# Kernel tuning notes

Measured on AMD Instinct MI355X. Metric: run time of the kernel, lower is better.

Reference implementation:

```python
import jax, jax.numpy as jnp
import numpy as np

NODE_TYPES = ["patient", "visit", "symptom", "procedure", "disease", "drug"]
N = {"patient": 20000, "visit": 100000, "symptom": 4000, "procedure": 8000,
     "disease": 10000, "drug": 4000}
D = 128          # embedding_dim == hidden_channels
N_LAYERS = 4     # conv1..conv4
# (src, dst) per relation; reverse edges included so every node type gets messages
REL = [("patient", "visit"), ("visit", "patient"),
       ("visit", "symptom"), ("symptom", "visit"),
       ("visit", "procedure"), ("procedure", "visit"),
       ("visit", "disease"), ("disease", "visit"),
       ("visit", "drug"), ("drug", "visit")]
E_FWD = {("patient", "visit"): 100000, ("visit", "symptom"): 300000,
         ("visit", "procedure"): 200000, ("visit", "disease"): 250000,
         ("visit", "drug"): 300000}
EI_NAMES = ["ei_pv", "ei_vp", "ei_vs", "ei_sv", "ei_vpr", "ei_prv",
            "ei_vd", "ei_dv", "ei_vdr", "ei_drv"]
E_LABEL = 200000


def setup_inputs() -> dict:
    key = jax.random.key(0)
    ks = iter(jax.random.split(key, 64))
    inp = {}
    for nt in NODE_TYPES:
        inp[f"node_id_{nt}"] = jnp.arange(N[nt], dtype=jnp.int32)
        inp[f"emb_{nt}"] = jax.random.normal(next(ks), (N[nt], D), jnp.float32)
    for name, (src, dst) in zip(EI_NAMES, REL):
        e = E_FWD.get((src, dst), E_FWD.get((dst, src)))
        row = jax.random.randint(next(ks), (e,), 0, N[src], dtype=jnp.int32)
        col = jax.random.randint(next(ks), (e,), 0, N[dst], dtype=jnp.int32)
        inp[name] = jnp.stack([row, col])
    R = len(REL)
    inp["W_l"] = jax.random.normal(next(ks), (N_LAYERS, R, D, D), jnp.float32) * 0.05
    inp["b_l"] = jnp.zeros((N_LAYERS, R, D), jnp.float32)
    inp["W_r"] = jax.random.normal(next(ks), (N_LAYERS, R, D, D), jnp.float32) * 0.05
    inp["cls_w1"] = jax.random.normal(next(ks), (2 * D, D), jnp.float32) * 0.05
    inp["cls_b1"] = jnp.zeros((D,), jnp.float32)
    inp["cls_w2"] = jax.random.normal(next(ks), (D, 1), jnp.float32) * 0.05
    inp["cls_b2"] = jnp.zeros((1,), jnp.float32)
    row = jax.random.randint(next(ks), (E_LABEL,), 0, N["visit"], dtype=jnp.int32)
    col = jax.random.randint(next(ks), (E_LABEL,), 0, N["drug"], dtype=jnp.int32)
    inp["edge_label_index"] = jnp.stack([row, col])
    inp["edge_label"] = jax.random.bernoulli(next(ks), 0.5, (E_LABEL,)).astype(jnp.float32)
    return inp


def _hetero_sage_layer(x, eis, Wl, bl, Wr):
    # to_hetero semantics: out[dst] = sum over edge types (src,rel,dst) of
    #   SAGEConv_rel: lin_l(mean_j x[src][j]) + lin_r(x[dst])   (PyG defaults)
    out = {nt: jnp.zeros_like(v) for nt, v in x.items()}
    for r, (src, dst) in enumerate(REL):
        ei = eis[r]
        n_dst = x[dst].shape[0]
        msg = jax.ops.segment_sum(x[src][ei[0]], ei[1], num_segments=n_dst)
        deg = jax.ops.segment_sum(jnp.ones((ei.shape[1],), x[src].dtype), ei[1],
                                  num_segments=n_dst)
        mean = msg / jnp.maximum(deg, 1.0)[:, None]  # empty segments stay 0 as in PyG
        out[dst] = out[dst] + mean @ Wl[r] + bl[r] + x[dst] @ Wr[r]
    return out


def reference(node_id_patient, node_id_visit, node_id_symptom, node_id_procedure,
              node_id_disease, node_id_drug,
              emb_patient, emb_visit, emb_symptom, emb_procedure, emb_disease, emb_drug,
              ei_pv, ei_vp, ei_vs, ei_sv, ei_vpr, ei_prv, ei_vd, ei_dv, ei_vdr, ei_drv,
              W_l, b_l, W_r, cls_w1, cls_b1, cls_w2, cls_b2,
              edge_label_index, edge_label):
    x = {"patient": emb_patient[node_id_patient],
         "visit": emb_visit[node_id_visit],
         "symptom": emb_symptom[node_id_symptom],
         "procedure": emb_procedure[node_id_procedure],
         "disease": emb_disease[node_id_disease],
         "drug": emb_drug[node_id_drug]}
    eis = [ei_pv, ei_vp, ei_vs, ei_sv, ei_vpr, ei_prv, ei_vd, ei_dv, ei_vdr, ei_drv]
    for l in range(N_LAYERS):
        x = _hetero_sage_layer(x, eis, W_l[l], b_l[l], W_r[l])
        if l < N_LAYERS - 1:  # relu after conv1..conv3 only; dropout is eval-mode identity
            x = {k: jax.nn.relu(v) for k, v in x.items()}
    # Classifier: gather visit/drug node features per labeled edge, concat, MLP
    zv = x["visit"][edge_label_index[0]]
    zd = x["drug"][edge_label_index[1]]
    h = jax.nn.relu(jnp.concatenate([zv, zd], axis=-1) @ cls_w1 + cls_b1)
    pred = (h @ cls_w2 + cls_b2).reshape(-1)
    # BCE with logits: softplus(z) - z*y, mean-reduced
    loss = jnp.mean(jax.nn.softplus(pred) - pred * edge_label)
    return loss, pred
```

## Files before the change

### kernel.cpp

```cpp
#include <hip/hip_runtime.h>
#include <cmath>


typedef _Float16 f16x8 __attribute__((ext_vector_type(8)));
typedef float f32x4 __attribute__((ext_vector_type(4)));

#define NREL 10
#define NCOUNTS 546000
#define NEDGES  2300000
#define NVISIT  100000
#define NVEDGES 1150000
#define PLW 546816
#define WT_ELEMS (4 * PLW + 69632)
#define XELEMS 18688000UL
#define SELEMS 5888000UL
#define NBKT 873
#define BCAP 5056

struct GatherMeta { const float* emb[6]; const int* nid[6]; int rows[6]; int off[6]; };
struct AggMeta { const int* rp[5]; _Float16* meanH[5]; _Float16* meanL[5]; int M[5]; };
struct BkMeta {
  const int* ei[NREL]; int E[NREL]; int cbc[NREL]; int ndst[NREL];
  int sh[NREL]; int bb[NREL]; int nb[NREL];
};
struct MTask {
  const _Float16* AH0; const _Float16* AL0;
  const _Float16* AH1; const _Float16* AL1;
  const _Float16* W;
  const float* bias;
  _Float16* outH; _Float16* outL;
  int M, blkOff, K, relu;
};
struct MMeta { MTask t[6]; int nTasks; };

__global__ __launch_bounds__(256) void conv0(GatherMeta g, _Float16* __restrict__ H,
                                             _Float16* __restrict__ L) {
  int t = blockIdx.y;
  int i = blockIdx.x * 256 + threadIdx.x;
  if (i >= g.rows[t] * 16) return;
  int row = i >> 4, q = i & 15;
  int s = g.nid[t][row];
  const float* p = g.emb[t] + (size_t)s * 128 + q * 8;
  float4 v0 = *(const float4*)p;
  float4 v1 = *(const float4*)(p + 4);
  float v[8] = {v0.x, v0.y, v0.z, v0.w, v1.x, v1.y, v1.z, v1.w};
  f16x8 h, l;
  #pragma unroll
  for (int j = 0; j < 8; ++j) {
    h[j] = (_Float16)v[j];
    l[j] = (_Float16)(v[j] - (float)h[j]);
  }
  size_t o = (size_t)(g.off[t] + row) * 128 + q * 8;
  *(f16x8*)(H + o) = h;
  *(f16x8*)(L + o) = l;
}

__global__ __launch_bounds__(256) void bkt_p1(BkMeta bm, int* __restrict__ bcur,
                                              int* __restrict__ bdata) {
  __shared__ int cnt[128];
  __shared__ int base[128];
  __shared__ unsigned short rnk[4096];
  int r = blockIdx.y;
  int E = bm.E[r], sh = bm.sh[r], bb = bm.bb[r], nb = bm.nb[r];
  int tid = threadIdx.x;
  if (tid < 128) cnt[tid] = 0;
  __syncthreads();
  int e0 = blockIdx.x * 4096;
  if (e0 >= E) return;
  const int* dstp = bm.ei[r] + E;
  const int* srcp = bm.ei[r];
  #pragma unroll
  for (int i = 0; i < 16; ++i) {
    int e = e0 + i * 256 + tid;
    if (e < E) {
      int b = dstp[e] >> sh;
      rnk[i * 256 + tid] = (unsigned short)atomicAdd(&cnt[b], 1);
    }
  }
  __syncthreads();
  if (tid < nb && cnt[tid] > 0) base[tid] = atomicAdd(&bcur[bb + tid], cnt[tid]);
  __syncthreads();
  #pragma unroll
  for (int i = 0; i < 16; ++i) {
    int e = e0 + i * 256 + tid;
    if (e < E) {
      int d = dstp[e];
      int b = d >> sh;
      int pos = base[b] + (int)rnk[i * 256 + tid];
      if (pos < BCAP)
        bdata[(size_t)(bb + b) * BCAP + pos] = ((d & ((1 << sh) - 1)) << 17) | srcp[e];
    }
  }
}

__global__ __launch_bounds__(256) void bkt_p2a(BkMeta bm, const int* __restrict__ bcur,
                                               const int* __restrict__ bdata,
                                               int* __restrict__ counts) {
  __shared__ int hist[2048];
  int g = blockIdx.x;
  int r = 0;
  #pragma unroll
  for (int i = 1; i < NREL; ++i) if (g >= bm.bb[i]) r = i;
  int lb = g - bm.bb[r];
  int sh = bm.sh[r], dpb = 1 << sh;
  int tid = threadIdx.x;
  for (int d = tid; d < dpb; d += 256) hist[d] = 0;
  __syncthreads();
  int cnt = bcur[g]; if (cnt > BCAP) cnt = BCAP;
  const int* bd = bdata + (size_t)g * BCAP;
  for (int i = tid; i < cnt; i += 256) atomicAdd(&hist[((unsigned)bd[i]) >> 17], 1);
  __syncthreads();
  int dBase = lb << sh;
  int dMax = bm.ndst[r] - dBase; if (dMax > dpb) dMax = dpb;
  for (int d = tid; d < dMax; d += 256) counts[bm.cbc[r] + dBase + d] = hist[d];
}

__global__ __launch_bounds__(1024) void scan1(const int* __restrict__ counts,
                                              int* __restrict__ partials) {
  __shared__ int s[1024];
  int i = blockIdx.x * 1024 + threadIdx.x;
  s[threadIdx.x] = (i < NCOUNTS) ? counts[i] : 0;
  __syncthreads();
  for (int off = 512; off > 0; off >>= 1) {
    if (threadIdx.x < off) s[threadIdx.x] += s[threadIdx.x + off];
    __syncthreads();
  }
  if (threadIdx.x == 0) partials[blockIdx.x] = s[0];
}

__global__ __launch_bounds__(1024) void scan2(int* __restrict__ partials, int nb) {
  __shared__ int s[1024];
  int t = threadIdx.x;
  int v = (t < nb) ? partials[t] : 0;
  s[t] = v;
  __syncthreads();
  for (int off = 1; off < 1024; off <<= 1) {
    int add = (t >= off) ? s[t - off] : 0;
    __syncthreads();
    s[t] += add;
    __syncthreads();
  }
  if (t < nb) partials[t] = s[t] - v;
}

__global__ __launch_bounds__(1024) void scan3(const int* __restrict__ counts,
                                              int* __restrict__ prefix,
                                              const int* __restrict__ partials) {
  __shared__ int s[1024];
  int t = threadIdx.x;
  int i = blockIdx.x * 1024 + t;
  int v = (i < NCOUNTS) ? counts[i] : 0;
  s[t] = v;
  __syncthreads();
  for (int off = 1; off < 1024; off <<= 1) {
    int add = (t >= off) ? s[t - off] : 0;
    __syncthreads();
    s[t] += add;
    __syncthreads();
  }
  int P = partials[blockIdx.x] + s[t] - v;
  if (i < NCOUNTS) prefix[i] = P;
  if (blockIdx.x == 0 && t == 0) prefix[NCOUNTS] = NEDGES;
}

__global__ __launch_bounds__(256) void bkt_p2b(BkMeta bm, const int* __restrict__ bcur,
                                               const int* __restrict__ bdata,
                                               const int* __restrict__ prefix,
                                               int* __restrict__ esrc) {
  __shared__ int pk[BCAP];
  __shared__ int srt[BCAP];
  __shared__ int cur[2048];
  __shared__ int part[256];
  __shared__ int baseSh;
  int g = blockIdx.x;
  int r = 0;
  #pragma unroll
  for (int i = 1; i < NREL; ++i) if (g >= bm.bb[i]) r = i;
  int lb = g - bm.bb[r];
  int sh = bm.sh[r], dpb = 1 << sh;
  int tid = threadIdx.x;
  int cnt = bcur[g]; if (cnt > BCAP) cnt = BCAP;
  const int* bd = bdata + (size_t)g * BCAP;
  for (int d = tid; d < dpb; d += 256) cur[d] = 0;
  for (int i = tid; i < cnt; i += 256) pk[i] = bd[i];
  __syncthreads();
  for (int i = tid; i < cnt; i += 256) atomicAdd(&cur[((unsigned)pk[i]) >> 17], 1);
  __syncthreads();
  int seg = (dpb + 255) >> 8;
  int s = 0;
  int b0 = tid * seg;
  for (int j = 0; j < seg; ++j) {
    int idx = b0 + j;
    if (idx < dpb) { int v = cur[idx]; cur[idx] = s; s += v; }
  }
  part[tid] = s;
  __syncthreads();
  for (int off = 1; off < 256; off <<= 1) {
    int add = (tid >= off) ? part[tid - off] : 0;
    __syncthreads();
    part[tid] += add;
    __syncthreads();
  }
  int myoff = part[tid] - s;
  for (int j = 0; j < seg; ++j) {
    int idx = b0 + j;
    if (idx < dpb) cur[idx] += myoff;
  }
  if (tid == 0) baseSh = prefix[bm.cbc[r] + (lb << sh)];
  __syncthreads();
  for (int i = tid; i < cnt; i += 256) {
    int p = pk[i];
    int pos = atomicAdd(&cur[((unsigned)p) >> 17], 1);
    srt[pos] = p & 0x1FFFF;
  }
  __syncthreads();
  int base = baseSh;
  for (int i = tid; i < cnt; i += 256) esrc[base + i] = srt[i];
}

__global__ __launch_bounds__(256) void merge_visit(const int* __restrict__ prefix,
                                                   const int* __restrict__ esrc,
                                                   int* __restrict__ mprefix,
                                                   int2* __restrict__ mesrc) {
  const int cbc[5]  = {0, 124000, 232000, 342000, 446000};
  const int yoff[5] = {0, 20000, 24000, 32000, 42000};
  int v = blockIdx.x * 256 + threadIdx.x;
  if (v >= NVISIT) return;
  int e0[5], e1[5];
  int base = 0;
  #pragma unroll
  for (int q = 0; q < 5; ++q) {
    e0[q] = prefix[cbc[q] + v];
    e1[q] = prefix[cbc[q] + v + 1];
    base += e0[q] - prefix[cbc[q]];
  }
  mprefix[v] = base;
  if (v == NVISIT - 1) {
    int t = base;
    #pragma unroll
    for (int q = 0; q < 5; ++q) t += e1[q] - e0[q];
    mprefix[NVISIT] = t;
  }
  int pos = base;
  #pragma unroll
  for (int q = 0; q < 5; ++q) {
    int d = e1[q] - e0[q];
    if (d > 0) {
      int wb = __float_as_int(1.f / (float)d);
      for (int e = e0[q]; e < e1[q]; ++e)
        mesrc[pos++] = make_int2(yoff[q] + esrc[e], wb);
    }
  }
}

__global__ __launch_bounds__(256) void prep_split(
    const float* __restrict__ W_l, const float* __restrict__ b_l,
    const float* __restrict__ W_r, const float* __restrict__ cw1,
    _Float16* __restrict__ Wt, float* __restrict__ visitSumB) {
  const int visitRel[5] = {0, 3, 5, 7, 9};
  const int inRel[5] = {1, 2, 4, 6, 8};
  int gid = blockIdx.x * 256 + threadIdx.x;
  if (gid < 1048576) {
    int l = gid >> 18, o = gid & 262143;
    float val; size_t base; int n, k, Kpad;
    if (o < 163840) {
      int t = o >> 15, e = o & 32767;
      k = e >> 7; n = e & 127; Kpad = 264;
      int r = inRel[t];
      val = (k < 128) ? W_l[(size_t)(l * 10 + r) * 16384 + k * 128 + n]
                      : W_r[(size_t)(l * 10 + r) * 16384 + (k - 128) * 128 + n];
      base = (size_t)l * PLW + t * 67584;
    } else if (o < 245760) {
      int q = (o - 163840) >> 14, e = (o - 163840) & 16383;
      k = e >> 7; n = e & 127; Kpad = 136;
      val = W_l[(size_t)(l * 10 + visitRel[q]) * 16384 + k * 128 + n];
      base = (size_t)l * PLW + 337920 + q * 34816;
    } else {
      int e = o - 245760;
      k = e >> 7; n = e & 127; Kpad = 136;
      val = 0.f;
      #pragma unroll
      for (int q = 0; q < 5; ++q)
        val += W_r[(size_t)(l * 10 + visitRel[q]) * 16384 + k * 128 + n];
      base = (size_t)l * PLW + 512000;
    }
    _Float16 h = (_Float16)val;
    _Float16 lo = (_Float16)(val - (float)h);
    Wt[base + (size_t)n * Kpad + k] = h;
    Wt[base + (size_t)(128 + n) * Kpad + k] = lo;
  } else if (gid < 1081344) {
    int e = gid - 1048576;
    int k = e >> 7, n = e & 127;
    float val = cw1[(size_t)k * 128 + n];
    _Float16 h = (_Float16)val;
    _Float16 lo = (_Float16)(val - (float)h);
    size_t base = (size_t)4 * PLW + (k < 128 ? 0 : 34816);
    int kk = k & 127;
    Wt[base + (size_t)n * 136 + kk] = h;
    Wt[base + (size_t)(128 + n) * 136 + kk] = lo;
  } else if (gid < 1081856) {
    int e = gid - 1081344;
    int l = e >> 7, c = e & 127;
    float val = 0.f;
    #pragma unroll
    for (int q = 0; q < 5; ++q) val += b_l[(l * 10 + visitRel[q]) * 128 + c];
    visitSumB[e] = val;
  }
}

__global__ __launch_bounds__(256) void agg_small(AggMeta m,
                                                 const _Float16* __restrict__ xvH,
                                                 const int* __restrict__ esrc) {
  int t = blockIdx.y;
  int row = blockIdx.x * 16 + (threadIdx.x >> 4);
  if (row >= m.M[t]) return;
  int q = threadIdx.x & 15;
  const int* rp = m.rp[t];
  int e0 = rp[row], e1 = rp[row + 1];
  float a[8];
  #pragma unroll
  for (int j = 0; j < 8; ++j) a[j] = 0.f;
  int e = e0;
  for (; e + 4 <= e1; e += 4) {
    int s0 = esrc[e], s1 = esrc[e + 1], s2 = esrc[e + 2], s3 = esrc[e + 3];
    f16x8 v0 = *(const f16x8*)(xvH + (size_t)s0 * 128 + q * 8);
    f16x8 v1 = *(const f16x8*)(xvH + (size_t)s1 * 128 + q * 8);
    f16x8 v2 = *(const f16x8*)(xvH + (size_t)s2 * 128 + q * 8);
    f16x8 v3 = *(const f16x8*)(xvH + (size_t)s3 * 128 + q * 8);
    #pragma unroll
    for (int j = 0; j < 8; ++j)
      a[j] += ((float)v0[j] + (float)v1[j]) + ((float)v2[j] + (float)v3[j]);
  }
  for (; e < e1; ++e) {
    int s = esrc[e];
    f16x8 v = *(const f16x8*)(xvH + (size_t)s * 128 + q * 8);
    #pragma unroll
    for (int j = 0; j < 8; ++j) a[j] += (float)v[j];
  }
  float inv = (e1 > e0) ? 1.f / (float)(e1 - e0) : 0.f;
  f16x8 h, l;
  #pragma unroll
  for (int j = 0; j < 8; ++j) {
    float v = a[j] * inv;
    h[j] = (_Float16)v;
    l[j] = (_Float16)(v - (float)h[j]);
  }
  size_t o = (size_t)row * 128 + q * 8;
  *(f16x8*)(m.meanH[t] + o) = h;
  *(f16x8*)(m.meanL[t] + o) = l;
}

__global__ __launch_bounds__(256) void agg_visit(const int* __restrict__ mprefix,
                                                 const int2* __restrict__ mesrc,
                                                 const _Float16* __restrict__ YH,
                                                 _Float16* __restrict__ xvH,
                                                 _Float16* __restrict__ xvL, int doRelu) {
  int row = blockIdx.x * 16 + (threadIdx.x >> 4);
  if (row >= NVISIT) return;
  int q = threadIdx.x & 15;
  size_t o = (size_t)row * 128 + q * 8;
  f16x8 h0 = *(f16x8*)(xvH + o);
  f16x8 l0 = *(f16x8*)(xvL + o);
  float a[8];
  #pragma unroll
  for (int j = 0; j < 8; ++j) a[j] = (float)h0[j] + (float)l0[j];
  int e0 = mprefix[row], e1 = mprefix[row + 1];
  int e = e0;
  for (; e + 4 <= e1; e += 4) {
    int2 p0 = mesrc[e], p1 = mesrc[e + 1], p2 = mesrc[e + 2], p3 = mesrc[e + 3];
    f16x8 v0 = *(const f16x8*)(YH + (size_t)p0.x * 128 + q * 8);
    f16x8 v1 = *(const f16x8*)(YH + (size_t)p1.x * 128 + q * 8);
    f16x8 v2 = *(const f16x8*)(YH + (size_t)p2.x * 128 + q * 8);
    f16x8 v3 = *(const f16x8*)(YH + (size_t)p3.x * 128 + q * 8);
    float w0 = __int_as_float(p0.y), w1 = __int_as_float(p1.y);
    float w2 = __int_as_float(p2.y), w3 = __int_as_float(p3.y);
    #pragma unroll
    for (int j = 0; j < 8; ++j)
      a[j] += (w0 * (float)v0[j] + w1 * (float)v1[j]) +
              (w2 * (float)v2[j] + w3 * (float)v3[j]);
  }
  for (; e < e1; ++e) {
    int2 p = mesrc[e];
    f16x8 v = *(const f16x8*)(YH + (size_t)p.x * 128 + q * 8);
    float w = __int_as_float(p.y);
    #pragma unroll
    for (int j = 0; j < 8; ++j) a[j] += w * (float)v[j];
  }
  f16x8 h, l;
  #pragma unroll
  for (int j = 0; j < 8; ++j) {
    float v = doRelu ? fmaxf(a[j], 0.f) : a[j];
    h[j] = (_Float16)v;
    l[j] = (_Float16)(v - (float)h[j]);
  }
  *(f16x8*)(xvH + o) = h;
  *(f16x8*)(xvL + o) = l;
}

__global__ __launch_bounds__(256, 2) void mgemm(MMeta mm) {
  int b = blockIdx.x;
  int ti = 0;
  for (int i = 1; i < mm.nTasks; ++i) if (b >= mm.t[i].blkOff) ti = i;
  MTask tk = mm.t[ti];
  int blockRow = (b - tk.blkOff) * 128;
  int Kpad = tk.K + 8;

  __shared__ _Float16 Ash[2][128][72];
  int tid = threadIdx.x;
  int wave = tid >> 6, lane = tid & 63;
  int quad = lane >> 4, lm = lane & 15;
  int wr = wave >> 1, wc = wave & 1;

  f32x4 acc[4][4];
  #pragma unroll
  for (int i = 0; i < 4; ++i)
    #pragma unroll
    for (int j = 0; j < 4; ++j) acc[i][j] = (f32x4){0.f, 0.f, 0.f, 0.f};

  const _Float16* wrowH[4];
  const _Float16* wrowL[4];
  #pragma unroll
  for (int nt = 0; nt < 4; ++nt) {
    int n = wc * 64 + nt * 16 + lm;
    wrowH[nt] = tk.W + (size_t)n * Kpad;
    wrowL[nt] = tk.W + (size_t)(128 + n) * Kpad;
  }

  int sr = tid >> 1, sk = (tid & 1) * 32;
  int gr = blockRow + sr; if (gr >= tk.M) gr = tk.M - 1;
  for (int k0 = 0; k0 < tk.K; k0 += 64) {
    const _Float16* AH = (k0 < 128) ? tk.AH0 : tk.AH1;
    const _Float16* AL = (k0 < 128) ? tk.AL0 : tk.AL1;
    size_t abase = (size_t)gr * 128 + (k0 & 127) + sk;
    #pragma unroll
    for (int c = 0; c < 4; ++c) {
      *(f16x8*)&Ash[0][sr][sk + c * 8] = *(const f16x8*)(AH + abase + c * 8);
      *(f16x8*)&Ash[1][sr][sk + c * 8] = *(const f16x8*)(AL + abase + c * 8);
    }
    __syncthreads();
    #pragma unroll
    for (int ks = 0; ks < 64; ks += 32) {
      int kf = k0 + ks + quad * 8;
      f16x8 bh[4], bl[4];
      #pragma unroll
      for (int nt = 0; nt < 4; ++nt) {
        bh[nt] = *(const f16x8*)(wrowH[nt] + kf);
        bl[nt] = *(const f16x8*)(wrowL[nt] + kf);
      }
      #pragma unroll
      for (int mt = 0; mt < 4; ++mt) {
        int r = wr * 64 + mt * 16 + lm;
        f16x8 ah = *(const f16x8*)&Ash[0][r][ks + quad * 8];
        f16x8 al = *(const f16x8*)&Ash[1][r][ks + quad * 8];
        #pragma unroll
        for (int nt = 0; nt < 4; ++nt) {
          acc[mt][nt] = __builtin_amdgcn_mfma_f32_16x16x32_f16(ah, bh[nt], acc[mt][nt], 0, 0, 0);
          acc[mt][nt] = __builtin_amdgcn_mfma_f32_16x16x32_f16(ah, bl[nt], acc[mt][nt], 0, 0, 0);
          acc[mt][nt] = __builtin_amdgcn_mfma_f32_16x16x32_f16(al, bh[nt], acc[mt][nt], 0, 0, 0);
        }
      }
    }
    __syncthreads();
  }

  float bv[4];
  #pragma unroll
  for (int nt = 0; nt < 4; ++nt)
    bv[nt] = tk.bias ? tk.bias[wc * 64 + nt * 16 + lm] : 0.f;
  #pragma unroll
  for (int mt = 0; mt < 4; ++mt) {
    #pragma unroll
    for (int i = 0; i < 4; ++i) {
      int grow = blockRow + wr * 64 + mt * 16 + quad * 4 + i;
      if (grow >= tk.M) continue;
      size_t ob = (size_t)grow * 128 + wc * 64 + lm;
      #pragma unroll
      for (int nt = 0; nt < 4; ++nt) {
        float v = acc[mt][nt][i] + bv[nt];
        if (tk.relu) v = fmaxf(v, 0.f);
        _Float16 h = (_Float16)v;
        tk.outH[ob + nt * 16] = h;
        if (tk.outL) tk.outL[ob + nt * 16] = (_Float16)(v - (float)h);
      }
    }
  }
}

__global__ __launch_bounds__(256) void cls_edge(
    const _Float16* __restrict__ UH, const _Float16* __restrict__ UL,
    const _Float16* __restrict__ VH, const _Float16* __restrict__ VL,
    const int* __restrict__ eli, const float* __restrict__ w2,
    const float* __restrict__ b2, const float* __restrict__ y,
    float* __restrict__ lossOut, float* __restrict__ pred, int M) {
  __shared__ float lsum[4];
  int tid = threadIdx.x;
  int q = tid & 15;
  int lane = tid & 63;
  float w2v[8];
  #pragma unroll
  for (int j = 0; j < 8; ++j) w2v[j] = w2[q * 8 + j];
  float bias = b2[0];
  float lacc = 0.f;
  int e0 = blockIdx.x * 128 + (tid >> 4);
  #pragma unroll
  for (int p = 0; p < 8; ++p) {
    int e = e0 + p * 16;
    if (e < M) {
      int vi = eli[e], di = eli[M + e];
      size_t uo = (size_t)vi * 128 + q * 8;
      size_t vo = (size_t)di * 128 + q * 8;
      f16x8 uh = *(const f16x8*)(UH + uo);
      f16x8 ul = *(const f16x8*)(UL + uo);
      f16x8 vh = *(const f16x8*)(VH + vo);
      f16x8 vl = *(const f16x8*)(VL + vo);
      float part = 0.f;
      #pragma unroll
      for (int j = 0; j < 8; ++j) {
        float t = ((float)uh[j] + (float)ul[j]) + ((float)vh[j] + (float)vl[j]);
        part += fmaxf(t, 0.f) * w2v[j];
      }
      part += __shfl_xor(part, 1);
      part += __shfl_xor(part, 2);
      part += __shfl_xor(part, 4);
      part += __shfl_xor(part, 8);
      if (q == 0) {
        float z = part + bias;
        pred[e] = z;
        lacc += fmaxf(z, 0.f) + log1pf(expf(-fabsf(z))) - z * y[e];
      }
    }
  }
  lacc += __shfl_xor(lacc, 16);
  lacc += __shfl_xor(lacc, 32);
  if (lane == 0) lsum[tid >> 6] = lacc;
  __syncthreads();
  if (tid == 0)
    atomicAdd(lossOut, (lsum[0] + lsum[1] + lsum[2] + lsum[3]) * (1.0f / 200000.0f));
}

extern "C" void kernel_launch(void* const* d_in, const int* in_sizes, int n_in,
                              void* d_out, int out_size, void* d_ws, size_t ws_size,
                              hipStream_t stream) {
  static const int kRows[6] = {20000, 100000, 4000, 8000, 10000, 4000};
  static const int kOff[6]  = {0, 20000, 120000, 124000, 132000, 142000};
  static const int kSmallT[5]   = {0, 2, 3, 4, 5};
  static const int kInRel[5]    = {1, 2, 4, 6, 8};
  static const int kCbcIn[5]    = {100000, 120000, 224000, 332000, 442000};
  static const int kYOff[5]     = {0, 20000, 24000, 32000, 42000};
  static const int kBOff[5]     = {0, 157, 189, 252, 331};
  static const int kCbcA[NREL]  = {0, 100000, 120000, 124000, 224000,
                                   232000, 332000, 342000, 442000, 446000};
  static const int kEhA[NREL]   = {100000, 100000, 300000, 300000, 200000,
                                   200000, 250000, 250000, 300000, 300000};
  static const int kNdst[NREL]  = {100000, 20000, 4000, 100000, 8000,
                                   100000, 10000, 100000, 4000, 100000};
  static const int kSh[NREL]    = {11, 9, 5, 10, 7, 10, 7, 10, 5, 10};
  static const int kNB[NREL]    = {49, 40, 125, 98, 63, 98, 79, 98, 125, 98};
  static const int kBB[NREL]    = {0, 49, 89, 214, 312, 375, 473, 552, 650, 775};

  const float* W_l = (const float*)d_in[22];
  const float* b_l = (const float*)d_in[23];
  const float* W_r = (const float*)d_in[24];
  const float* cw1 = (const float*)d_in[25];
  const float* cb1 = (const float*)d_in[26];
  const float* cw2 = (const float*)d_in[27];
  const float* cb2 = (const float*)d_in[28];
  const int* eli = (const int*)d_in[29];
  const float* ylab = (const float*)d_in[30];

  _Float16* H = (_Float16*)d_ws;
  _Float16* L = H + XELEMS;
  _Float16* meanH = L + XELEMS;
  _Float16* meanL = meanH + SELEMS;
  _Float16* YH = meanL + SELEMS;
  _Float16* Wt = YH + SELEMS;
  int* prefix = (int*)(Wt + WT_ELEMS);
  int* counts = prefix + 546004;
  int* esrc = counts + NCOUNTS;
  int* partials = esrc + NEDGES;
  float* visitSumB = (float*)(partials + 1024);
  int* bcur = (int*)(visitSumB + 512);
  int* bdata = bcur + 1024;

  int* mprefix = counts;
  int2* mesrc = (int2*)bdata;

  _Float16* UH = meanH;
  _Float16* VH = meanH + (size_t)NVISIT * 128;
  _Float16* VL = VH + (size_t)4000 * 128;
  _Float16* UL = (_Float16*)prefix;

  BkMeta bm;
  for (int r = 0; r < NREL; ++r) {
    bm.ei[r] = (const int*)d_in[12 + r];
    bm.E[r] = kEhA[r];
    bm.cbc[r] = kCbcA[r];
    bm.ndst[r] = kNdst[r];
    bm.sh[r] = kSh[r];
    bm.bb[r] = kBB[r];
    bm.nb[r] = kNB[r];
  }

  hipMemsetAsync(bcur, 0, NBKT * sizeof(int), stream);
  hipMemsetAsync(d_out, 0, sizeof(float), stream);

  prep_split<<<(1081856 + 255) / 256, 256, 0, stream>>>(W_l, b_l, W_r, cw1, Wt, visitSumB);

  GatherMeta gm;
  for (int t = 0; t < 6; ++t) {
    gm.nid[t] = (const int*)d_in[2 * t];
    gm.emb[t] = (const float*)d_in[2 * t + 1];
    gm.rows[t] = kRows[t];
    gm.off[t] = kOff[t];
  }
  conv0<<<dim3(6250, 6), 256, 0, stream>>>(gm, H, L);

  bkt_p1<<<dim3(74, NREL), 256, 0, stream>>>(bm, bcur, bdata);
  bkt_p2a<<<dim3(NBKT), 256, 0, stream>>>(bm, bcur, bdata, counts);
  scan1<<<534, 1024, 0, stream>>>(counts, partials);
  scan2<<<1, 1024, 0, stream>>>(partials, 534);
  scan3<<<534, 1024, 0, stream>>>(counts, prefix, partials);
  bkt_p2b<<<dim3(NBKT), 256, 0, stream>>>(bm, bcur, bdata, prefix, esrc);
  merge_visit<<<dim3((NVISIT + 255) / 256), 256, 0, stream>>>(prefix, esrc, mprefix, mesrc);

  _Float16* xvH = H + (size_t)kOff[1] * 128;
  _Float16* xvL = L + (size_t)kOff[1] * 128;

  for (int l = 0; l < 4; ++l) {
    int doRelu = (l < 3);
    int last = (l == 3);
    _Float16* LW = Wt + (size_t)l * PLW;

    AggMeta am;
    if (!last) {
      for (int t = 0; t < 5; ++t) {
        am.rp[t] = prefix + kCbcIn[t];
        am.meanH[t] = meanH + (size_t)kYOff[t] * 128;
        am.meanL[t] = meanL + (size_t)kYOff[t] * 128;
        am.M[t] = kRows[kSmallT[t]];
      }
      agg_small<<<dim3(1250, 5), 256, 0, stream>>>(am, xvH, esrc);
    } else {
      am.rp[0] = prefix + kCbcIn[4];
      am.meanH[0] = meanH + (size_t)kYOff[4] * 128;
      am.meanL[0] = meanL + (size_t)kYOff[4] * 128;
      am.M[0] = 4000;
      agg_small<<<dim3(250, 1), 256, 0, stream>>>(am, xvH, esrc);
    }

    MMeta m2;
    m2.nTasks = 6;
    for (int q = 0; q < 5; ++q) {
      size_t so = (size_t)kOff[kSmallT[q]] * 128;
      m2.t[q].AH0 = H + so; m2.t[q].AL0 = L + so;
      m2.t[q].AH1 = nullptr; m2.t[q].AL1 = nullptr;
      m2.t[q].W = LW + 337920 + (size_t)q * 34816;
      m2.t[q].bias = nullptr;
      m2.t[q].outH = YH + (size_t)kYOff[q] * 128;
      m2.t[q].outL = nullptr;
      m2.t[q].M = kRows[kSmallT[q]];
      m2.t[q].blkOff = kBOff[q];
      m2.t[q].K = 128;
      m2.t[q].relu = 0;
    }
    m2.t[5].AH0 = xvH; m2.t[5].AL0 = xvL;
    m2.t[5].AH1 = nullptr; m2.t[5].AL1 = nullptr;
    m2.t[5].W = LW + 512000;
    m2.t[5].bias = visitSumB + l * 128;
    m2.t[5].outH = xvH; m2.t[5].outL = xvL;
    m2.t[5].M = NVISIT;
    m2.t[5].blkOff = 363;
    m2.t[5].K = 128;
    m2.t[5].relu = 0;
    mgemm<<<dim3(363 + 782), 256, 0, stream>>>(m2);

    MMeta m1;
    if (!last) {
      m1.nTasks = 5;
      for (int t = 0; t < 5; ++t) {
        size_t mo = (size_t)kYOff[t] * 128;
        size_t so = (size_t)kOff[kSmallT[t]] * 128;
        m1.t[t].AH0 = meanH + mo; m1.t[t].AL0 = meanL + mo;
        m1.t[t].AH1 = H + so;     m1.t[t].AL1 = L + so;
        m1.t[t].W = LW + (size_t)t * 67584;
        m1.t[t].bias = b_l + (size_t)(l * 10 + kInRel[t]) * 128;
        m1.t[t].outH = H + so;    m1.t[t].outL = L + so;
        m1.t[t].M = kRows[kSmallT[t]];
        m1.t[t].blkOff = kBOff[t];
        m1.t[t].K = 256;
        m1.t[t].relu = doRelu;
      }
      mgemm<<<dim3(363), 256, 0, stream>>>(m1);
    } else {
      size_t mo = (size_t)kYOff[4] * 128;
      size_t so = (size_t)kOff[5] * 128;
      m1.nTasks = 1;
      m1.t[0].AH0 = meanH + mo; m1.t[0].AL0 = meanL + mo;
      m1.t[0].AH1 = H + so;     m1.t[0].AL1 = L + so;
      m1.t[0].W = LW + (size_t)4 * 67584;
      m1.t[0].bias = b_l + (size_t)(l * 10 + kInRel[4]) * 128;
      m1.t[0].outH = H + so;    m1.t[0].outL = L + so;
      m1.t[0].M = 4000;
      m1.t[0].blkOff = 0;
      m1.t[0].K = 256;
      m1.t[0].relu = 0;
      mgemm<<<dim3(32), 256, 0, stream>>>(m1);
    }

    agg_visit<<<dim3(6250), 256, 0, stream>>>(mprefix, mesrc, YH, xvH, xvL, doRelu);
  }

  MMeta muv;
  muv.nTasks = 2;
  muv.t[0].AH0 = xvH; muv.t[0].AL0 = xvL;
  muv.t[0].AH1 = nullptr; muv.t[0].AL1 = nullptr;
  muv.t[0].W = Wt + (size_t)4 * PLW;
  muv.t[0].bias = cb1;
  muv.t[0].outH = UH; muv.t[0].outL = UL;
  muv.t[0].M = NVISIT;
  muv.t[0].blkOff = 0;
  muv.t[0].K = 128;
  muv.t[0].relu = 0;
  muv.t[1].AH0 = H + (size_t)kOff[5] * 128; muv.t[1].AL0 = L + (size_t)kOff[5] * 128;
  muv.t[1].AH1 = nullptr; muv.t[1].AL1 = nullptr;
  muv.t[1].W = Wt + (size_t)4 * PLW + 34816;
  muv.t[1].bias = nullptr;
  muv.t[1].outH = VH; muv.t[1].outL = VL;
  muv.t[1].M = 4000;
  muv.t[1].blkOff = 782;
  muv.t[1].K = 128;
  muv.t[1].relu = 0;
  mgemm<<<dim3(782 + 32), 256, 0, stream>>>(muv);

  const int ML = 200000;
  cls_edge<<<dim3((ML + 127) / 128), 256, 0, stream>>>(
      UH, UL, VH, VL, eli, cw2, cb2, ylab,
      (float*)d_out, (float*)d_out + 1, ML);
}
```

Measured before the change: 943.0 us.

## Fuse small-type aggregation with message GEMM; merge visit self-GEMM into update launch

```diff
diff --git a/kernel.cpp b/kernel.cpp
--- a/kernel.cpp
+++ b/kernel.cpp
@@ -18,7 +18,6 @@
 #define BCAP 5056
 
 struct GatherMeta { const float* emb[6]; const int* nid[6]; int rows[6]; int off[6]; };
-struct AggMeta { const int* rp[5]; _Float16* meanH[5]; _Float16* meanL[5]; int M[5]; };
 struct BkMeta {
   const int* ei[NREL]; int E[NREL]; int cbc[NREL]; int ndst[NREL];
   int sh[NREL]; int bb[NREL]; int nb[NREL];
@@ -32,6 +31,12 @@
   int M, blkOff, K, relu;
 };
 struct MMeta { MTask t[6]; int nTasks; };
+struct F1Meta {
+  const int* rp[5]; _Float16* mH[5]; _Float16* mL[5]; int aM[5]; int aOff[5];
+  int nAgg; int aggTotal;
+  const _Float16* gAH[5]; const _Float16* gAL[5]; const _Float16* gW[5];
+  _Float16* gY[5]; int gM[5]; int gOff[5]; int nG;
+};
 
 __global__ __launch_bounds__(256) void conv0(GatherMeta g, _Float16* __restrict__ H,
                                              _Float16* __restrict__ L) {
@@ -308,46 +313,92 @@
   }
 }
 
-__global__ __launch_bounds__(256) void agg_small(AggMeta m,
+__global__ __launch_bounds__(256, 8) void fused1(F1Meta f,
                                                  const _Float16* __restrict__ xvH,
                                                  const int* __restrict__ esrc) {
-  int t = blockIdx.y;
-  int row = blockIdx.x * 16 + (threadIdx.x >> 4);
-  if (row >= m.M[t]) return;
-  int q = threadIdx.x & 15;
-  const int* rp = m.rp[t];
-  int e0 = rp[row], e1 = rp[row + 1];
-  float a[8];
-  #pragma unroll
-  for (int j = 0; j < 8; ++j) a[j] = 0.f;
-  int e = e0;
-  for (; e + 4 <= e1; e += 4) {
-    int s0 = esrc[e], s1 = esrc[e + 1], s2 = esrc[e + 2], s3 = esrc[e + 3];
-    f16x8 v0 = *(const f16x8*)(xvH + (size_t)s0 * 128 + q * 8);
-    f16x8 v1 = *(const f16x8*)(xvH + (size_t)s1 * 128 + q * 8);
-    f16x8 v2 = *(const f16x8*)(xvH + (size_t)s2 * 128 + q * 8);
-    f16x8 v3 = *(const f16x8*)(xvH + (size_t)s3 * 128 + q * 8);
-    #pragma unroll
-    for (int j = 0; j < 8; ++j)
-      a[j] += ((float)v0[j] + (float)v1[j]) + ((float)v2[j] + (float)v3[j]);
-  }
-  for (; e < e1; ++e) {
-    int s = esrc[e];
-    f16x8 v = *(const f16x8*)(xvH + (size_t)s * 128 + q * 8);
-    #pragma unroll
-    for (int j = 0; j < 8; ++j) a[j] += (float)v[j];
-  }
-  float inv = (e1 > e0) ? 1.f / (float)(e1 - e0) : 0.f;
-  f16x8 h, l;
-  #pragma unroll
-  for (int j = 0; j < 8; ++j) {
-    float v = a[j] * inv;
-    h[j] = (_Float16)v;
-    l[j] = (_Float16)(v - (float)h[j]);
-  }
-  size_t o = (size_t)row * 128 + q * 8;
-  *(f16x8*)(m.meanH[t] + o) = h;
-  *(f16x8*)(m.meanL[t] + o) = l;
+  int b = blockIdx.x;
+  int tid = threadIdx.x;
+  if (b < f.aggTotal) {
+    int t = 0;
+    #pragma unroll
+    for (int i = 1; i < 5; ++i) if (i < f.nAgg && b >= f.aOff[i]) t = i;
+    int row = (b - f.aOff[t]) * 16 + (tid >> 4);
+    if (row >= f.aM[t]) return;
+    int q = tid & 15;
+    const int* rp = f.rp[t];
+    int e0 = rp[row], e1 = rp[row + 1];
+    float a[8];
+    #pragma unroll
+    for (int j = 0; j < 8; ++j) a[j] = 0.f;
+    int e = e0;
+    for (; e + 4 <= e1; e += 4) {
+      int s0 = esrc[e], s1 = esrc[e + 1], s2 = esrc[e + 2], s3 = esrc[e + 3];
+      f16x8 v0 = *(const f16x8*)(xvH + (size_t)s0 * 128 + q * 8);
+      f16x8 v1 = *(const f16x8*)(xvH + (size_t)s1 * 128 + q * 8);
+      f16x8 v2 = *(const f16x8*)(xvH + (size_t)s2 * 128 + q * 8);
+      f16x8 v3 = *(const f16x8*)(xvH + (size_t)s3 * 128 + q * 8);
+      #pragma unroll
+      for (int j = 0; j < 8; ++j)
+        a[j] += ((float)v0[j] + (float)v1[j]) + ((float)v2[j] + (float)v3[j]);
+    }
+    for (; e < e1; ++e) {
+      int s = esrc[e];
+      f16x8 v = *(const f16x8*)(xvH + (size_t)s * 128 + q * 8);
+      #pragma unroll
+      for (int j = 0; j < 8; ++j) a[j] += (float)v[j];
+    }
+    float inv = (e1 > e0) ? 1.f / (float)(e1 - e0) : 0.f;
+    f16x8 h, l;
+    #pragma unroll
+    for (int j = 0; j < 8; ++j) {
+      float v = a[j] * inv;
+      h[j] = (_Float16)v;
+      l[j] = (_Float16)(v - (float)h[j]);
+    }
+    size_t o = (size_t)row * 128 + q * 8;
+    *(f16x8*)(f.mH[t] + o) = h;
+    *(f16x8*)(f.mL[t] + o) = l;
+    return;
+  }
+  b -= f.aggTotal;
+  int g = 0;
+  #pragma unroll
+  for (int i = 1; i < 5; ++i) if (i < f.nG && b >= f.gOff[i]) g = i;
+  int blockRow = (b - f.gOff[g]) * 32;
+  int lane = tid & 63, wave = tid >> 6;
+  int quad = lane >> 4, lm = lane & 15;
+  int wr = wave >> 1, wc = wave & 1;
+  const _Float16* AH = f.gAH[g];
+  const _Float16* AL = f.gAL[g];
+  const _Float16* W = f.gW[g];
+  int M = f.gM[g];
+  int ar = blockRow + wr * 16 + lm;
+  if (ar >= M) ar = M - 1;
+  f32x4 acc[4];
+  #pragma unroll
+  for (int nt = 0; nt < 4; ++nt) acc[nt] = (f32x4){0.f, 0.f, 0.f, 0.f};
+  for (int ks = 0; ks < 128; ks += 32) {
+    f16x8 ah = *(const f16x8*)(AH + (size_t)ar * 128 + ks + quad * 8);
+    f16x8 al = *(const f16x8*)(AL + (size_t)ar * 128 + ks + quad * 8);
+    #pragma unroll
+    for (int nt = 0; nt < 4; ++nt) {
+      int n = wc * 64 + nt * 16 + lm;
+      f16x8 bh = *(const f16x8*)(W + (size_t)n * 136 + ks + quad * 8);
+      f16x8 bl = *(const f16x8*)(W + (size_t)(128 + n) * 136 + ks + quad * 8);
+      acc[nt] = __builtin_amdgcn_mfma_f32_16x16x32_f16(ah, bh, acc[nt], 0, 0, 0);
+      acc[nt] = __builtin_amdgcn_mfma_f32_16x16x32_f16(ah, bl, acc[nt], 0, 0, 0);
+      acc[nt] = __builtin_amdgcn_mfma_f32_16x16x32_f16(al, bh, acc[nt], 0, 0, 0);
+    }
+  }
+  _Float16* Y = f.gY[g];
+  #pragma unroll
+  for (int i = 0; i < 4; ++i) {
+    int grow = blockRow + wr * 16 + quad * 4 + i;
+    if (grow >= M) continue;
+    #pragma unroll
+    for (int nt = 0; nt < 4; ++nt)
+      Y[(size_t)grow * 128 + wc * 64 + nt * 16 + lm] = (_Float16)acc[nt][i];
+  }
 }
 
 __global__ __launch_bounds__(256) void agg_visit(const int* __restrict__ mprefix,
@@ -548,6 +599,9 @@
   static const int kCbcIn[5]    = {100000, 120000, 224000, 332000, 442000};
   static const int kYOff[5]     = {0, 20000, 24000, 32000, 42000};
   static const int kBOff[5]     = {0, 157, 189, 252, 331};
+  static const int kAggOff[5]   = {0, 1250, 1500, 2000, 2625};
+  static const int kLeanOff[5]  = {0, 625, 750, 1000, 1313};
+  const int kAggTotal = 2875, kLeanTotal = 1438;
   static const int kCbcA[NREL]  = {0, 100000, 120000, 124000, 224000,
                                    232000, 332000, 342000, 442000, 446000};
   static const int kEhA[NREL]   = {100000, 100000, 300000, 300000, 200000,
@@ -631,80 +685,88 @@
     int last = (l == 3);
     _Float16* LW = Wt + (size_t)l * PLW;
 
-    AggMeta am;
+    F1Meta f1;
     if (!last) {
       for (int t = 0; t < 5; ++t) {
-        am.rp[t] = prefix + kCbcIn[t];
-        am.meanH[t] = meanH + (size_t)kYOff[t] * 128;
-        am.meanL[t] = meanL + (size_t)kYOff[t] * 128;
-        am.M[t] = kRows[kSmallT[t]];
+        f1.rp[t] = prefix + kCbcIn[t];
+        f1.mH[t] = meanH + (size_t)kYOff[t] * 128;
+        f1.mL[t] = meanL + (size_t)kYOff[t] * 128;
+        f1.aM[t] = kRows[kSmallT[t]];
+        f1.aOff[t] = kAggOff[t];
       }
-      agg_small<<<dim3(1250, 5), 256, 0, stream>>>(am, xvH, esrc);
+      f1.nAgg = 5;
+      f1.aggTotal = kAggTotal;
     } else {
-      am.rp[0] = prefix + kCbcIn[4];
-      am.meanH[0] = meanH + (size_t)kYOff[4] * 128;
-      am.meanL[0] = meanL + (size_t)kYOff[4] * 128;
-      am.M[0] = 4000;
-      agg_small<<<dim3(250, 1), 256, 0, stream>>>(am, xvH, esrc);
-    }
-
-    MMeta m2;
-    m2.nTasks = 6;
+      f1.rp[0] = prefix + kCbcIn[4];
+      f1.mH[0] = meanH + (size_t)kYOff[4] * 128;
+      f1.mL[0] = meanL + (size_t)kYOff[4] * 128;
+      f1.aM[0] = 4000;
+      f1.aOff[0] = 0;
+      for (int t = 1; t < 5; ++t) { f1.rp[t] = nullptr; f1.mH[t] = nullptr; f1.mL[t] = nullptr; f1.aM[t] = 0; f1.aOff[t] = 0; }
+      f1.nAgg = 1;
+      f1.aggTotal = 250;
+    }
     for (int q = 0; q < 5; ++q) {
       size_t so = (size_t)kOff[kSmallT[q]] * 128;
-      m2.t[q].AH0 = H + so; m2.t[q].AL0 = L + so;
-      m2.t[q].AH1 = nullptr; m2.t[q].AL1 = nullptr;
-      m2.t[q].W = LW + 337920 + (size_t)q * 34816;
-      m2.t[q].bias = nullptr;
-      m2.t[q].outH = YH + (size_t)kYOff[q] * 128;
-      m2.t[q].outL = nullptr;
-      m2.t[q].M = kRows[kSmallT[q]];
-      m2.t[q].blkOff = kBOff[q];
-      m2.t[q].K = 128;
-      m2.t[q].relu = 0;
-    }
-    m2.t[5].AH0 = xvH; m2.t[5].AL0 = xvL;
-    m2.t[5].AH1 = nullptr; m2.t[5].AL1 = nullptr;
-    m2.t[5].W = LW + 512000;
-    m2.t[5].bias = visitSumB + l * 128;
-    m2.t[5].outH = xvH; m2.t[5].outL = xvL;
-    m2.t[5].M = NVISIT;
-    m2.t[5].blkOff = 363;
-    m2.t[5].K = 128;
-    m2.t[5].relu = 0;
-    mgemm<<<dim3(363 + 782), 256, 0, stream>>>(m2);
-
-    MMeta m1;
+      f1.gAH[q] = H + so;
+      f1.gAL[q] = L + so;
+      f1.gW[q] = LW + 337920 + (size_t)q * 34816;
+      f1.gY[q] = YH + (size_t)kYOff[q] * 128;
+      f1.gM[q] = kRows[kSmallT[q]];
+      f1.gOff[q] = kLeanOff[q];
+    }
+    f1.nG = 5;
+    fused1<<<dim3(f1.aggTotal + kLeanTotal), 256, 0, stream>>>(f1, xvH, esrc);
+
+    MMeta m;
     if (!last) {
-      m1.nTasks = 5;
+      m.nTasks = 6;
       for (int t = 0; t < 5; ++t) {
         size_t mo = (size_t)kYOff[t] * 128;
         size_t so = (size_t)kOff[kSmallT[t]] * 128;
-        m1.t[t].AH0 = meanH + mo; m1.t[t].AL0 = meanL + mo;
-        m1.t[t].AH1 = H + so;     m1.t[t].AL1 = L + so;
-        m1.t[t].W = LW + (size_t)t * 67584;
-        m1.t[t].bias = b_l + (size_t)(l * 10 + kInRel[t]) * 128;
-        m1.t[t].outH = H + so;    m1.t[t].outL = L + so;
-        m1.t[t].M = kRows[kSmallT[t]];
-        m1.t[t].blkOff = kBOff[t];
-        m1.t[t].K = 256;
-        m1.t[t].relu = doRelu;
+        m.t[t].AH0 = meanH + mo; m.t[t].AL0 = meanL + mo;
+        m.t[t].AH1 = H + so;     m.t[t].AL1 = L + so;
+        m.t[t].W = LW + (size_t)t * 67584;
+        m.t[t].bias = b_l + (size_t)(l * 10 + kInRel[t]) * 128;
+        m.t[t].outH = H + so;    m.t[t].outL = L + so;
+        m.t[t].M = kRows[kSmallT[t]];
+        m.t[t].blkOff = kBOff[t];
+        m.t[t].K = 256;
+        m.t[t].relu = doRelu;
       }
-      mgemm<<<dim3(363), 256, 0, stream>>>(m1);
+      m.t[5].AH0 = xvH; m.t[5].AL0 = xvL;
+      m.t[5].AH1 = nullptr; m.t[5].AL1 = nullptr;
+      m.t[5].W = LW + 512000;
+      m.t[5].bias = visitSumB + l * 128;
+      m.t[5].outH = xvH; m.t[5].outL = xvL;
+      m.t[5].M = NVISIT;
+      m.t[5].blkOff = 363;
+      m.t[5].K = 128;
+      m.t[5].relu = 0;
+      mgemm<<<dim3(363 + 782), 256, 0, stream>>>(m);
     } else {
       size_t mo = (size_t)kYOff[4] * 128;
       size_t so = (size_t)kOff[5] * 128;
-      m1.nTasks = 1;
-      m1.t[0].AH0 = meanH + mo; m1.t[0].AL0 = meanL + mo;
-      m1.t[0].AH1 = H + so;     m1.t[0].AL1 = L + so;
-      m1.t[0].W = LW + (size_t)4 * 67584;
-      m1.t[0].bias = b_l + (size_t)(l * 10 + kInRel[4]) * 128;
-      m1.t[0].outH = H + so;    m1.t[0].outL = L + so;
-      m1.t[0].M = 4000;
-      m1.t[0].blkOff = 0;
-      m1.t[0].K = 256;
-      m1.t[0].relu = 0;
-      mgemm<<<dim3(32), 256, 0, stream>>>(m1);
+      m.nTasks = 2;
+      m.t[0].AH0 = meanH + mo; m.t[0].AL0 = meanL + mo;
+      m.t[0].AH1 = H + so;     m.t[0].AL1 = L + so;
+      m.t[0].W = LW + (size_t)4 * 67584;
+      m.t[0].bias = b_l + (size_t)(l * 10 + kInRel[4]) * 128;
+      m.t[0].outH = H + so;    m.t[0].outL = L + so;
+      m.t[0].M = 4000;
+      m.t[0].blkOff = 0;
+      m.t[0].K = 256;
+      m.t[0].relu = 0;
+      m.t[1].AH0 = xvH; m.t[1].AL0 = xvL;
+      m.t[1].AH1 = nullptr; m.t[1].AL1 = nullptr;
+      m.t[1].W = LW + 512000;
+      m.t[1].bias = visitSumB + l * 128;
+      m.t[1].outH = xvH; m.t[1].outL = xvL;
+      m.t[1].M = NVISIT;
+      m.t[1].blkOff = 32;
+      m.t[1].K = 128;
+      m.t[1].relu = 0;
+      mgemm<<<dim3(32 + 782), 256, 0, stream>>>(m);
     }
 
     agg_visit<<<dim3(6250), 256, 0, stream>>>(mprefix, mesrc, YH, xvH, xvL, doRelu);
```

Result: faster. 911.0 us (-3.4%).
